# Kernel optimization log

Measured on AMD Instinct MI355X. Metric: run time of the kernel, lower is better.

The kernel has to match this reference:

```python
import jax, jax.numpy as jnp
import numpy as np

# dims: B batch, S src len, D input_size, H rnn hidden, E embedding_dim,
# V = output_size + 2 (vocab + Start/End), T = max target len (+2 for Start/End)
B, S, D, H, E, V, T = 128, 512, 256, 512, 256, 1002, 34
END = V - 1  # 'End' token index


def _gru_layer(x, h0, Wih, Whh, bih, bhh):
    """PyTorch-convention GRU layer. x: [B,T,Din], h0: [B,H].
    Wih: [3H,Din], Whh: [3H,H]. Returns (outputs [B,T,H], h_T [B,H])."""
    def step(h, xt):
        gi = xt @ Wih.T + bih            # [B,3H]
        gh = h @ Whh.T + bhh             # [B,3H]
        i_r, i_z, i_n = jnp.split(gi, 3, axis=-1)
        h_r, h_z, h_n = jnp.split(gh, 3, axis=-1)
        r = jax.nn.sigmoid(i_r + h_r)
        z = jax.nn.sigmoid(i_z + h_z)
        n = jnp.tanh(i_n + r * h_n)
        h_new = (1.0 - z) * n + z * h
        return h_new, h_new
    hT, ys = jax.lax.scan(step, h0, jnp.swapaxes(x, 0, 1))
    return jnp.swapaxes(ys, 0, 1), hT


def _gru_stack(x, h0s, layers):
    """h0s: [L,B,H]; layers: list of (Wih,Whh,bih,bhh). Returns (out, h [L,B,H])."""
    hs = []
    y = x
    for l, (Wih, Whh, bih, bhh) in enumerate(layers):
        y, hT = _gru_layer(y, h0s[l], Wih, Whh, bih, bhh)
        hs.append(hT)
    return y, jnp.stack(hs, axis=0)


def setup_inputs() -> dict:
    key = jax.random.key(0)
    ks = jax.random.split(key, 32)
    sc = 0.05
    inp = {}
    inp['source'] = jax.random.normal(ks[0], (B, S, D), dtype=jnp.float32)
    inp['target_ids'] = jax.random.randint(ks[1], (B, T), 0, V)
    inp['lengths'] = jax.random.randint(ks[2], (B,), 2, T + 1)
    inp['emb'] = sc * jax.random.normal(ks[3], (V, E), dtype=jnp.float32)
    # encoder layer 0 (in=D) and layer 1 (in=H)
    inp['enc_Wih0'] = sc * jax.random.normal(ks[4], (3 * H, D), dtype=jnp.float32)
    inp['enc_Whh0'] = sc * jax.random.normal(ks[5], (3 * H, H), dtype=jnp.float32)
    inp['enc_bih0'] = jnp.zeros((3 * H,), jnp.float32)
    inp['enc_bhh0'] = jnp.zeros((3 * H,), jnp.float32)
    inp['enc_Wih1'] = sc * jax.random.normal(ks[6], (3 * H, H), dtype=jnp.float32)
    inp['enc_Whh1'] = sc * jax.random.normal(ks[7], (3 * H, H), dtype=jnp.float32)
    inp['enc_bih1'] = jnp.zeros((3 * H,), jnp.float32)
    inp['enc_bhh1'] = jnp.zeros((3 * H,), jnp.float32)
    # decoder layer 0 (in=E) and layer 1 (in=H)
    inp['dec_Wih0'] = sc * jax.random.normal(ks[8], (3 * H, E), dtype=jnp.float32)
    inp['dec_Whh0'] = sc * jax.random.normal(ks[9], (3 * H, H), dtype=jnp.float32)
    inp['dec_bih0'] = jnp.zeros((3 * H,), jnp.float32)
    inp['dec_bhh0'] = jnp.zeros((3 * H,), jnp.float32)
    inp['dec_Wih1'] = sc * jax.random.normal(ks[10], (3 * H, H), dtype=jnp.float32)
    inp['dec_Whh1'] = sc * jax.random.normal(ks[11], (3 * H, H), dtype=jnp.float32)
    inp['dec_bih1'] = jnp.zeros((3 * H,), jnp.float32)
    inp['dec_bhh1'] = jnp.zeros((3 * H,), jnp.float32)
    # fc: H -> 5H -> 2H -> V
    inp['fc_W1'] = sc * jax.random.normal(ks[12], (5 * H, H), dtype=jnp.float32)
    inp['fc_b1'] = jnp.zeros((5 * H,), jnp.float32)
    inp['fc_W2'] = sc * jax.random.normal(ks[13], (2 * H, 5 * H), dtype=jnp.float32)
    inp['fc_b2'] = jnp.zeros((2 * H,), jnp.float32)
    inp['fc_W3'] = sc * jax.random.normal(ks[14], (V, 2 * H), dtype=jnp.float32)
    inp['fc_b3'] = jnp.zeros((V,), jnp.float32)
    return inp


def reference(source, target_ids, lengths, emb,
              enc_Wih0, enc_Whh0, enc_bih0, enc_bhh0,
              enc_Wih1, enc_Whh1, enc_bih1, enc_bhh1,
              dec_Wih0, dec_Whh0, dec_bih0, dec_bhh0,
              dec_Wih1, dec_Whh1, dec_bih1, dec_bhh1,
              fc_W1, fc_b1, fc_W2, fc_b2, fc_W3, fc_b3):
    Bx = source.shape[0]
    h0 = jnp.zeros((2, Bx, H), source.dtype)
    # encoder: only final hidden state h [L,B,H] is used
    _, h = _gru_stack(source, h0,
                      [(enc_Wih0, enc_Whh0, enc_bih0, enc_bhh0),
                       (enc_Wih1, enc_Whh1, enc_bih1, enc_bhh1)])
    # decoder over embedded (Start + target + End + pad) sequences
    tg = emb[target_ids]                               # [B,T,E]
    out, _ = _gru_stack(tg, h,
                        [(dec_Wih0, dec_Whh0, dec_bih0, dec_bhh0),
                         (dec_Wih1, dec_Whh1, dec_bih1, dec_bhh1)])
    # pad_packed_sequence zeroes timesteps >= length; sum over time
    mask = (jnp.arange(T)[None, :] < lengths[:, None]).astype(out.dtype)  # [B,T]
    pooled = jnp.einsum('bth,bt->bh', out, mask)       # [B,H]
    x = pooled @ fc_W1.T + fc_b1
    x = x @ fc_W2.T + fc_b2
    x = x @ fc_W3.T + fc_b3
    scores = jax.nn.sigmoid(x)                         # [B,V]
    # CrossEntropyLoss against the 'End' index for every row
    logp = jax.nn.log_softmax(scores, axis=-1)
    loss = -jnp.mean(logp[:, END])
    return loss
```

## Files before the change

kernel.cpp:

```cpp
#include <hip/hip_runtime.h>
#include <hip/hip_bf16.h>
#include <math.h>

#define B_ 128
#define S_ 512
#define D_ 256
#define H_ 512
#define E_ 256
#define V_ 1002
#define T_ 34
#define END_ 1001
#define NWG_TOTAL 128
#define HROWB 1040
#define GPITCH 20

typedef __attribute__((ext_vector_type(8))) short short8;
typedef __attribute__((ext_vector_type(4))) float f32x4;
typedef __attribute__((ext_vector_type(4))) int i32x4;
typedef unsigned long long u64;

__device__ __forceinline__ float bf2f(unsigned short u){
  union { unsigned int i; float f; } x; x.i = ((unsigned int)u) << 16; return x.f;
}
__device__ __forceinline__ unsigned short f2bf(float f){
  union { float f; unsigned int i; } x; x.f = f;
  unsigned int r = x.i + 0x7fffu + ((x.i >> 16) & 1u);
  return (unsigned short)(r >> 16);
}
__device__ __forceinline__ float sigm(float x){ return 1.0f / (1.0f + expf(-x)); }

__device__ __forceinline__ void store_coh8(unsigned short* p, u64 v){
  __hip_atomic_store((u64*)p, v, __ATOMIC_RELAXED, __HIP_MEMORY_SCOPE_AGENT);
}

__device__ __forceinline__ i32x4 load_flags16(const unsigned* p){
  i32x4 r;
  asm volatile("global_load_dwordx4 %0, %1, off sc0 sc1\n\ts_waitcnt vmcnt(0)"
               : "=v"(r) : "v"(p) : "memory");
  return r;
}

__device__ __forceinline__ void stage_tile_coh(const unsigned short* src, char* dst, int tid){
  i32x4 r[16];
  #pragma unroll
  for (int p = 0; p < 16; ++p){
    const char* sp = (const char*)src + p * 4096 + tid * 16;
    asm volatile("global_load_dwordx4 %0, %1, off sc0 sc1" : "=v"(r[p]) : "v"(sp));
  }
  asm volatile("s_waitcnt vmcnt(0)" ::: "memory");
  #pragma unroll
  for (int p = 0; p < 16; ++p){
    const int off = p * 4096 + tid * 16;
    *reinterpret_cast<i32x4*>(dst + (off >> 10) * HROWB + (off & 1023)) = r[p];
  }
}


__global__ void f2bf_kernel(const float* __restrict__ in, unsigned short* __restrict__ out, int n){
  int i = blockIdx.x * blockDim.x + threadIdx.x;
  int stride = gridDim.x * blockDim.x;
  for (; i < n; i += stride) out[i] = f2bf(in[i]);
}

__global__ void embed_kernel(const float* __restrict__ emb, const int* __restrict__ ids,
                             unsigned short* __restrict__ out){
  int i = blockIdx.x * blockDim.x + threadIdx.x;
  if (i >= B_ * T_ * E_) return;
  int bt = i >> 8;
  int e  = i & (E_ - 1);
  out[i] = f2bf(emb[(size_t)ids[bt] * E_ + e]);
}

__global__ void build_wcat(const float* __restrict__ Wih, const float* __restrict__ Whh,
                           unsigned short* __restrict__ Wcat, int Din){
  int K = Din + H_;
  int total = 2048 * K;
  int i = blockIdx.x * blockDim.x + threadIdx.x;
  int stride = gridDim.x * blockDim.x;
  for (; i < total; i += stride){
    int n = i / K, k = i - n * K;
    int g = n >> 9, j = n & 511;
    float v;
    if (g < 2){
      int r = (g << 9) + j;
      v = (k < Din) ? Wih[(size_t)r * Din + k] : Whh[(size_t)r * H_ + (k - Din)];
    } else if (g == 2){
      v = (k < Din) ? Wih[(size_t)(1024 + j) * Din + k] : 0.0f;
    } else {
      v = (k < Din) ? 0.0f : Whh[(size_t)(1024 + j) * H_ + (k - Din)];
    }
    Wcat[i] = f2bf(v);
  }
}

__global__ void build_bias(const float* __restrict__ bih, const float* __restrict__ bhh,
                           float* __restrict__ out){
  int j = blockIdx.x * blockDim.x + threadIdx.x;
  if (j >= 512) return;
  out[j]        = bih[j] + bhh[j];
  out[512 + j]  = bih[512 + j] + bhh[512 + j];
  out[1024 + j] = bih[1024 + j];
  out[1536 + j] = bhh[1024 + j];
}


template<int KT, int XKT>
__device__ __forceinline__ void run_layer(
    char* smem,
    const unsigned short* __restrict__ Wc, const float* __restrict__ bias4,
    const unsigned short* __restrict__ Xbase, int x_rs, int x_ts,
    unsigned short* Ybase,
    unsigned short* hb0, unsigned short* hb1,
    int T, unsigned round0,
    unsigned* own_flags, int slot,
    unsigned* prod_flags, unsigned prod0,
    u64* hprev,
    int jtile, int mh, int wv, int lane)
{
  constexpr int K   = KT * 32;
  constexpr int KTL = KT / 4;
  const int tid  = threadIdx.x;
  const int ln   = lane & 15;
  const int lk8  = (lane >> 4) << 3;
  const int base_m = mh * 64;
  const int q = wv;

  char*  hA   = smem;
  float* gbuf = (float*)(smem + 64 * HROWB);

  short8 wreg[4][KTL];
  #pragma unroll
  for (int g = 0; g < 4; ++g)
    #pragma unroll
    for (int k = 0; k < KTL; ++k)
      wreg[g][k] = *reinterpret_cast<const short8*>(
          Wc + (size_t)(g * 512 + jtile * 16 + ln) * K + (size_t)(q * KTL + k) * 32 + lk8);

  const int erow  = tid >> 2;
  const int ecol0 = (tid & 3) << 2;
  const int ej    = (jtile << 4) + ecol0;
  const int egr   = base_m + erow;
  f32x4 bR, bZ, bNI, bNH;
  #pragma unroll
  for (int c = 0; c < 4; ++c){
    bR[c]  = bias4[ej + c];
    bZ[c]  = bias4[512 + ej + c];
    bNI[c] = bias4[1024 + ej + c];
    bNH[c] = bias4[1536 + ej + c];
  }

  for (int t = 0; t < T; ++t){
    if (wv == 0){
      const unsigned own_t  = round0 + (unsigned)t;
      const unsigned prod_t = prod0 + (unsigned)t + 1u;
      const unsigned* pofs = own_flags + (lane & 7) * 4;
      const unsigned* ppfs = prod_flags ? (prod_flags + (lane & 7) * 4) : nullptr;
      for (;;){
        i32x4 f = load_flags16(pofs);
        bool ok = (unsigned)f.x >= own_t && (unsigned)f.y >= own_t &&
                  (unsigned)f.z >= own_t && (unsigned)f.w >= own_t;
        if (ppfs){
          i32x4 g = load_flags16(ppfs);
          ok = ok && (unsigned)g.x >= prod_t && (unsigned)g.y >= prod_t &&
                     (unsigned)g.z >= prod_t && (unsigned)g.w >= prod_t;
        }
        if (__all(ok)) break;
        __builtin_amdgcn_s_sleep(1);
      }
    }
    __syncthreads();

    const unsigned short* Hin  = (t & 1) ? hb1 : hb0;
    unsigned short*       Hout = (t & 1) ? hb0 : hb1;
    const unsigned short* Xt   = Xbase + (size_t)t * x_ts;

    stage_tile_coh(Hin + ((size_t)base_m << 9), hA, tid);
    __syncthreads();

    f32x4 acc[4][4];
    #pragma unroll
    for (int g = 0; g < 4; ++g)
      #pragma unroll
      for (int mt = 0; mt < 4; ++mt) acc[g][mt] = (f32x4){0.f, 0.f, 0.f, 0.f};

    #pragma unroll
    for (int k = 0; k < KTL; ++k){
      const int kt = q * KTL + k;
      short8 a[4];
      if (kt < XKT){
        #pragma unroll
        for (int mt = 0; mt < 4; ++mt)
          a[mt] = *reinterpret_cast<const short8*>(
              Xt + (size_t)(base_m + mt * 16 + ln) * x_rs + kt * 32 + lk8);
      } else {
        #pragma unroll
        for (int mt = 0; mt < 4; ++mt)
          a[mt] = *reinterpret_cast<const short8*>(
              hA + (mt * 16 + ln) * HROWB + ((kt - XKT) * 32 + lk8) * 2);
      }
      #pragma unroll
      for (int g = 0; g < 4; ++g)
        #pragma unroll
        for (int mt = 0; mt < 4; ++mt)
          acc[g][mt] = __builtin_amdgcn_mfma_f32_16x16x32_bf16(a[mt], wreg[g][k], acc[g][mt], 0, 0, 0);
    }

    #pragma unroll
    for (int g = 0; g < 4; ++g)
      #pragma unroll
      for (int mt = 0; mt < 4; ++mt){
        const int rl = mt * 16 + ((lane >> 4) << 2);
        #pragma unroll
        for (int i = 0; i < 4; ++i)
          gbuf[((q * 4 + g) * 64 + rl + i) * GPITCH + ln] = acc[g][mt][i];
      }
    __syncthreads();

    {
      f32x4 p0 = (f32x4){0.f,0.f,0.f,0.f}, p1 = p0, p2 = p0, p3 = p0;
      #pragma unroll
      for (int qq = 0; qq < 4; ++qq){
        p0 += *reinterpret_cast<const f32x4*>(gbuf + ((qq * 4 + 0) * 64 + erow) * GPITCH + ecol0);
        p1 += *reinterpret_cast<const f32x4*>(gbuf + ((qq * 4 + 1) * 64 + erow) * GPITCH + ecol0);
        p2 += *reinterpret_cast<const f32x4*>(gbuf + ((qq * 4 + 2) * 64 + erow) * GPITCH + ecol0);
        p3 += *reinterpret_cast<const f32x4*>(gbuf + ((qq * 4 + 3) * 64 + erow) * GPITCH + ecol0);
      }
      u64 hv = *hprev;
      u64 hb = 0;
      #pragma unroll
      for (int c = 0; c < 4; ++c){
        float rr = sigm(p0[c] + bR[c]);
        float zz = sigm(p1[c] + bZ[c]);
        float nn = tanhf(p2[c] + bNI[c] + rr * (p3[c] + bNH[c]));
        float hp = bf2f((unsigned short)(hv >> (16 * c)));
        float hn = (1.0f - zz) * nn + zz * hp;
        hb |= ((u64)f2bf(hn)) << (16 * c);
      }
      *hprev = hb;
      store_coh8(Hout + ((size_t)egr << 9) + ej, hb);
      if (Ybase)
        store_coh8(Ybase + (size_t)t * (B_ * H_) + ((size_t)egr << 9) + ej, hb);
    }

    asm volatile("s_waitcnt vmcnt(0)" ::: "memory");
    __syncthreads();
    if (tid == 0)
      __hip_atomic_store(own_flags + slot, round0 + (unsigned)t + 1u,
                         __ATOMIC_RELAXED, __HIP_MEMORY_SCOPE_AGENT);
  }
}

__global__ __launch_bounds__(256, 1)
void rnn_persistent(
    const unsigned short* __restrict__ src, const unsigned short* __restrict__ tg,
    const unsigned short* __restrict__ Wc_e0, const unsigned short* __restrict__ Wc_e1,
    const unsigned short* __restrict__ Wc_d0, const unsigned short* __restrict__ Wc_d1,
    const float* __restrict__ b_e0, const float* __restrict__ b_e1,
    const float* __restrict__ b_d0, const float* __restrict__ b_d1,
    unsigned short* h0a, unsigned short* h0b,
    unsigned short* h1a, unsigned short* h1b,
    unsigned short* y0, unsigned short* z0, unsigned short* y1,
    unsigned* flags)
{
  __shared__ __align__(16) char smem[64 * HROWB + 16 * 64 * GPITCH * 4];
  __builtin_amdgcn_fence(__ATOMIC_ACQUIRE, "agent");
  const int wg = blockIdx.x;
  const int layer = wg >> 6;
  const int gidx = wg & 63;
  const int jtile = gidx & 31, mh = gidx >> 5;
  const int wv = threadIdx.x >> 6, lane = threadIdx.x & 63;
  unsigned* own  = flags + (size_t)((layer << 1) | mh) * 64;
  unsigned* prod = flags + (size_t)mh * 64;
  u64 hprev = 0;
  if (layer == 0){
    run_layer<24, 8>(smem, Wc_e0, b_e0, src, S_ * D_, D_, y0,
                     h0a, h0b, S_, 0u, own, jtile, nullptr, 0u, &hprev,
                     jtile, mh, wv, lane);
    run_layer<24, 8>(smem, Wc_d0, b_d0, tg, T_ * E_, E_, z0,
                     h0a, h0b, T_, 512u, own, jtile, nullptr, 0u, &hprev,
                     jtile, mh, wv, lane);
  } else {
    run_layer<32, 16>(smem, Wc_e1, b_e1, y0, H_, B_ * H_, (unsigned short*)nullptr,
                      h1a, h1b, S_, 0u, own, jtile, prod, 0u, &hprev,
                      jtile, mh, wv, lane);
    run_layer<32, 16>(smem, Wc_d1, b_d1, z0, H_, B_ * H_, y1,
                      h1a, h1b, T_, 512u, own, jtile, prod, 512u, &hprev,
                      jtile, mh, wv, lane);
  }
}

__global__ __launch_bounds__(256)
void gemm_nt(const unsigned short* __restrict__ A, const unsigned short* __restrict__ W,
             const float* __restrict__ bias,
             unsigned short* __restrict__ outB, float* __restrict__ outF,
             int M, int N, int K, int act)
{
  const int w    = threadIdx.x >> 6;
  const int lane = threadIdx.x & 63;
  const int ln   = lane & 15;
  const int lk8  = (lane >> 4) << 3;
  const int row0 = blockIdx.y * 32;
  const int col0 = blockIdx.x * 256 + w * 64;

  f32x4 acc[2][4];
  #pragma unroll
  for (int a = 0; a < 2; a++)
    #pragma unroll
    for (int g = 0; g < 4; g++) acc[a][g] = (f32x4){0.f, 0.f, 0.f, 0.f};

  const unsigned short* arow0 = A + (size_t)(row0 + ln) * K;
  const unsigned short* arow1 = A + (size_t)(row0 + 16 + ln) * K;
  const unsigned short* wrow[4];
  int ncol[4];
  #pragma unroll
  for (int nt = 0; nt < 4; ++nt){
    int n = col0 + nt * 16 + ln;
    ncol[nt] = n;
    int nc = n < N ? n : (N - 1);
    wrow[nt] = W + (size_t)nc * K;
  }

  const int nk = K >> 5;
  for (int kt = 0; kt < nk; ++kt){
    const int k = (kt << 5) + lk8;
    short8 a0 = *reinterpret_cast<const short8*>(arow0 + k);
    short8 a1 = *reinterpret_cast<const short8*>(arow1 + k);
    #pragma unroll
    for (int nt = 0; nt < 4; ++nt){
      short8 bf = *reinterpret_cast<const short8*>(wrow[nt] + k);
      acc[0][nt] = __builtin_amdgcn_mfma_f32_16x16x32_bf16(a0, bf, acc[0][nt], 0, 0, 0);
      acc[1][nt] = __builtin_amdgcn_mfma_f32_16x16x32_bf16(a1, bf, acc[1][nt], 0, 0, 0);
    }
  }

  #pragma unroll
  for (int nt = 0; nt < 4; ++nt){
    const int n = ncol[nt];
    if (n >= N) continue;
    const float bv = bias ? bias[n] : 0.0f;
    #pragma unroll
    for (int mt = 0; mt < 2; ++mt){
      const int rbase = row0 + mt * 16 + ((lane >> 4) << 2);
      #pragma unroll
      for (int reg = 0; reg < 4; ++reg){
        const int row = rbase + reg;
        if (row >= M) continue;
        float v = acc[mt][nt][reg] + bv;
        if (act == 1) v = sigm(v);
        if (outB) outB[(size_t)row * N + n] = f2bf(v);
        if (outF) outF[(size_t)row * N + n] = v;
      }
    }
  }
}


__global__ void pool_kernel(const unsigned short* __restrict__ y1, const int* __restrict__ lengths,
                            unsigned short* __restrict__ pooled){
  int i = blockIdx.x * blockDim.x + threadIdx.x;
  if (i >= B_ * H_) return;
  int b = i >> 9;
  int j = i & (H_ - 1);
  int len = lengths[b]; if (len > T_) len = T_;
  float s = 0.0f;
  for (int t = 0; t < len; ++t) s += bf2f(y1[((size_t)t * B_ + b) * H_ + j]);
  pooled[i] = f2bf(s);
}

__global__ void loss_kernel(const float* __restrict__ scores, float* __restrict__ out){
  __shared__ float wsum[4];
  const int w = threadIdx.x >> 6;
  const int lane = threadIdx.x & 63;
  float acc = 0.0f;
  for (int b = w; b < B_; b += 4){
    const float* row = scores + (size_t)b * V_;
    float vals[16];
    float mx = -1e30f;
    #pragma unroll
    for (int i = 0; i < 16; ++i){
      int c = lane + i * 64;
      vals[i] = (c < V_) ? row[c] : -1e30f;
      mx = fmaxf(mx, vals[i]);
    }
    #pragma unroll
    for (int off = 32; off; off >>= 1) mx = fmaxf(mx, __shfl_xor(mx, off));
    float se = 0.0f;
    #pragma unroll
    for (int i = 0; i < 16; ++i){
      int c = lane + i * 64;
      if (c < V_) se += expf(vals[i] - mx);
    }
    #pragma unroll
    for (int off = 32; off; off >>= 1) se += __shfl_xor(se, off);
    float logp = row[END_] - (mx + logf(se));
    acc += logp;
  }
  if (lane == 0) wsum[w] = acc;
  __syncthreads();
  if (threadIdx.x == 0){
    out[0] = -(wsum[0] + wsum[1] + wsum[2] + wsum[3]) / (float)B_;
  }
}


extern "C" void kernel_launch(void* const* d_in, const int* in_sizes, int n_in,
                              void* d_out, int out_size, void* d_ws, size_t ws_size,
                              hipStream_t stream) {
  const float* source   = (const float*)d_in[0];
  const int*   tgt_ids  = (const int*)  d_in[1];
  const int*   lengths  = (const int*)  d_in[2];
  const float* emb      = (const float*)d_in[3];
  const float* eWih0 = (const float*)d_in[4],  *eWhh0 = (const float*)d_in[5];
  const float* ebih0 = (const float*)d_in[6],  *ebhh0 = (const float*)d_in[7];
  const float* eWih1 = (const float*)d_in[8],  *eWhh1 = (const float*)d_in[9];
  const float* ebih1 = (const float*)d_in[10], *ebhh1 = (const float*)d_in[11];
  const float* dWih0 = (const float*)d_in[12], *dWhh0 = (const float*)d_in[13];
  const float* dbih0 = (const float*)d_in[14], *dbhh0 = (const float*)d_in[15];
  const float* dWih1 = (const float*)d_in[16], *dWhh1 = (const float*)d_in[17];
  const float* dbih1 = (const float*)d_in[18], *dbhh1 = (const float*)d_in[19];
  const float* fcW1 = (const float*)d_in[20], *fcb1 = (const float*)d_in[21];
  const float* fcW2 = (const float*)d_in[22], *fcb2 = (const float*)d_in[23];
  const float* fcW3 = (const float*)d_in[24], *fcb3 = (const float*)d_in[25];

  char* p = (char*)d_ws;
  auto alloc = [&](size_t bytes) -> void* {
    void* r = (void*)p;
    p += (bytes + 255) & ~(size_t)255;
    return r;
  };

  unsigned short* src_bf = (unsigned short*)alloc((size_t)B_ * S_ * D_ * 2);
  unsigned short* tg_bf  = (unsigned short*)alloc((size_t)B_ * T_ * E_ * 2);
  unsigned short* y0_bf  = (unsigned short*)alloc((size_t)S_ * B_ * H_ * 2);
  unsigned short* z0d    = (unsigned short*)alloc((size_t)T_ * B_ * H_ * 2);
  unsigned short* y1d    = (unsigned short*)alloc((size_t)T_ * B_ * H_ * 2);
  unsigned short* h0a = (unsigned short*)alloc((size_t)B_ * H_ * 2);
  unsigned short* h0b = (unsigned short*)alloc((size_t)B_ * H_ * 2);
  unsigned short* h1a = (unsigned short*)alloc((size_t)B_ * H_ * 2);
  unsigned short* h1b = (unsigned short*)alloc((size_t)B_ * H_ * 2);
  unsigned short* Wc_e0 = (unsigned short*)alloc((size_t)2048 * 768  * 2);
  unsigned short* Wc_e1 = (unsigned short*)alloc((size_t)2048 * 1024 * 2);
  unsigned short* Wc_d0 = (unsigned short*)alloc((size_t)2048 * 768  * 2);
  unsigned short* Wc_d1 = (unsigned short*)alloc((size_t)2048 * 1024 * 2);
  float* bias_e0 = (float*)alloc(2048 * 4);
  float* bias_e1 = (float*)alloc(2048 * 4);
  float* bias_d0 = (float*)alloc(2048 * 4);
  float* bias_d1 = (float*)alloc(2048 * 4);
  unsigned short* fcW1b = (unsigned short*)alloc((size_t)2560 * 512  * 2);
  unsigned short* fcW2b = (unsigned short*)alloc((size_t)1024 * 2560 * 2);
  unsigned short* fcW3b = (unsigned short*)alloc((size_t)V_ * 1024 * 2);
  unsigned short* pooled = (unsigned short*)alloc((size_t)B_ * H_ * 2);
  unsigned short* x1_bf  = (unsigned short*)alloc((size_t)B_ * 2560 * 2);
  unsigned short* x2_bf  = (unsigned short*)alloc((size_t)B_ * 1024 * 2);
  float* scores = (float*)alloc((size_t)B_ * V_ * 4);
  unsigned* flags = (unsigned*)alloc(4 * 64 * 4);

  f2bf_kernel<<<8192, 256, 0, stream>>>(source, src_bf, B_ * S_ * D_);
  embed_kernel<<<(B_ * T_ * E_ + 255) / 256, 256, 0, stream>>>(emb, tgt_ids, tg_bf);
  build_wcat<<<2048, 256, 0, stream>>>(eWih0, eWhh0, Wc_e0, D_);
  build_wcat<<<2048, 256, 0, stream>>>(eWih1, eWhh1, Wc_e1, H_);
  build_wcat<<<2048, 256, 0, stream>>>(dWih0, dWhh0, Wc_d0, E_);
  build_wcat<<<2048, 256, 0, stream>>>(dWih1, dWhh1, Wc_d1, H_);
  build_bias<<<2, 256, 0, stream>>>(ebih0, ebhh0, bias_e0);
  build_bias<<<2, 256, 0, stream>>>(ebih1, ebhh1, bias_e1);
  build_bias<<<2, 256, 0, stream>>>(dbih0, dbhh0, bias_d0);
  build_bias<<<2, 256, 0, stream>>>(dbih1, dbhh1, bias_d1);
  f2bf_kernel<<<4096, 256, 0, stream>>>(fcW1, fcW1b, 2560 * 512);
  f2bf_kernel<<<4096, 256, 0, stream>>>(fcW2, fcW2b, 1024 * 2560);
  f2bf_kernel<<<4096, 256, 0, stream>>>(fcW3, fcW3b, V_ * 1024);

  hipMemsetAsync(h0a, 0, (size_t)B_ * H_ * 2, stream);
  hipMemsetAsync(h0b, 0, (size_t)B_ * H_ * 2, stream);
  hipMemsetAsync(h1a, 0, (size_t)B_ * H_ * 2, stream);
  hipMemsetAsync(h1b, 0, (size_t)B_ * H_ * 2, stream);
  hipMemsetAsync(flags, 0, 4 * 64 * 4, stream);

  rnn_persistent<<<NWG_TOTAL, 256, 0, stream>>>(
      src_bf, tg_bf, Wc_e0, Wc_e1, Wc_d0, Wc_d1,
      bias_e0, bias_e1, bias_d0, bias_d1,
      h0a, h0b, h1a, h1b, y0_bf, z0d, y1d, flags);

  pool_kernel<<<(B_ * H_ + 255) / 256, 256, 0, stream>>>(y1d, lengths, pooled);

  {
    dim3 g1((2560 + 255) / 256, B_ / 32);
    gemm_nt<<<g1, 256, 0, stream>>>(pooled, fcW1b, fcb1, x1_bf, (float*)nullptr,
                                    B_, 2560, 512, 0);
    dim3 g2((1024 + 255) / 256, B_ / 32);
    gemm_nt<<<g2, 256, 0, stream>>>(x1_bf, fcW2b, fcb2, x2_bf, (float*)nullptr,
                                    B_, 1024, 2560, 0);
    dim3 g3((V_ + 255) / 256, B_ / 32);
    gemm_nt<<<g3, 256, 0, stream>>>(x2_bf, fcW3b, fcb3, (unsigned short*)nullptr, scores,
                                    B_, V_, 1024, 1);
  }

  loss_kernel<<<1, 256, 0, stream>>>(scores, (float*)d_out);
}
```

Before: 4.387 ms.

## Store full hidden-state history and read recurrent state directly from global

Replaces the two ping-pong hidden buffers and separate layer-output buffers with one time-indexed history buffer per layer. Each timestep now writes one fresh location, which serves as both the next recurrent input and the layer output. Because every step reads addresses that were never read before, the MFMA loop can load the previous hidden state straight from global memory with ordinary loads. This removes the coherent LDS staging copy and one barrier per step, and the duplicate Y store is dropped. In exchange it uses much larger buffers and depends on plain loads not returning stale cached data.

```diff
diff --git a/kernel.cpp b/kernel.cpp
--- a/kernel.cpp
+++ b/kernel.cpp
@@ -11,7 +11,7 @@
 #define T_ 34
 #define END_ 1001
 #define NWG_TOTAL 128
-#define HROWB 1040
+#define BH (B_ * H_)
 #define GPITCH 20
 
 typedef __attribute__((ext_vector_type(8))) short short8;
@@ -38,21 +38,6 @@
   asm volatile("global_load_dwordx4 %0, %1, off sc0 sc1\n\ts_waitcnt vmcnt(0)"
                : "=v"(r) : "v"(p) : "memory");
   return r;
-}
-
-__device__ __forceinline__ void stage_tile_coh(const unsigned short* src, char* dst, int tid){
-  i32x4 r[16];
-  #pragma unroll
-  for (int p = 0; p < 16; ++p){
-    const char* sp = (const char*)src + p * 4096 + tid * 16;
-    asm volatile("global_load_dwordx4 %0, %1, off sc0 sc1" : "=v"(r[p]) : "v"(sp));
-  }
-  asm volatile("s_waitcnt vmcnt(0)" ::: "memory");
-  #pragma unroll
-  for (int p = 0; p < 16; ++p){
-    const int off = p * 4096 + tid * 16;
-    *reinterpret_cast<i32x4*>(dst + (off >> 10) * HROWB + (off & 1023)) = r[p];
-  }
 }
 
 
@@ -106,11 +91,11 @@
 
 template<int KT, int XKT>
 __device__ __forceinline__ void run_layer(
-    char* smem,
+    float* gbuf,
     const unsigned short* __restrict__ Wc, const float* __restrict__ bias4,
     const unsigned short* __restrict__ Xbase, int x_rs, int x_ts,
-    unsigned short* Ybase,
-    unsigned short* hb0, unsigned short* hb1,
+    const unsigned short* __restrict__ Hread,
+    unsigned short* Hwrite,
     int T, unsigned round0,
     unsigned* own_flags, int slot,
     unsigned* prod_flags, unsigned prod0,
@@ -124,9 +109,6 @@
   const int lk8  = (lane >> 4) << 3;
   const int base_m = mh * 64;
   const int q = wv;
-
-  char*  hA   = smem;
-  float* gbuf = (float*)(smem + 64 * HROWB);
 
   short8 wreg[4][KTL];
   #pragma unroll
@@ -170,12 +152,8 @@
     }
     __syncthreads();
 
-    const unsigned short* Hin  = (t & 1) ? hb1 : hb0;
-    unsigned short*       Hout = (t & 1) ? hb0 : hb1;
-    const unsigned short* Xt   = Xbase + (size_t)t * x_ts;
-
-    stage_tile_coh(Hin + ((size_t)base_m << 9), hA, tid);
-    __syncthreads();
+    const unsigned short* Xt  = Xbase + (size_t)t * x_ts;
+    const unsigned short* Hin = Hread + (size_t)t * BH;
 
     f32x4 acc[4][4];
     #pragma unroll
@@ -196,7 +174,7 @@
         #pragma unroll
         for (int mt = 0; mt < 4; ++mt)
           a[mt] = *reinterpret_cast<const short8*>(
-              hA + (mt * 16 + ln) * HROWB + ((kt - XKT) * 32 + lk8) * 2);
+              Hin + (size_t)(base_m + mt * 16 + ln) * H_ + (kt - XKT) * 32 + lk8);
       }
       #pragma unroll
       for (int g = 0; g < 4; ++g)
@@ -237,9 +215,7 @@
         hb |= ((u64)f2bf(hn)) << (16 * c);
       }
       *hprev = hb;
-      store_coh8(Hout + ((size_t)egr << 9) + ej, hb);
-      if (Ybase)
-        store_coh8(Ybase + (size_t)t * (B_ * H_) + ((size_t)egr << 9) + ej, hb);
+      store_coh8(Hwrite + (size_t)t * BH + ((size_t)egr << 9) + ej, hb);
     }
 
     asm volatile("s_waitcnt vmcnt(0)" ::: "memory");
@@ -257,12 +233,10 @@
     const unsigned short* __restrict__ Wc_d0, const unsigned short* __restrict__ Wc_d1,
     const float* __restrict__ b_e0, const float* __restrict__ b_e1,
     const float* __restrict__ b_d0, const float* __restrict__ b_d1,
-    unsigned short* h0a, unsigned short* h0b,
-    unsigned short* h1a, unsigned short* h1b,
-    unsigned short* y0, unsigned short* z0, unsigned short* y1,
+    unsigned short* H0, unsigned short* H1,
     unsigned* flags)
 {
-  __shared__ __align__(16) char smem[64 * HROWB + 16 * 64 * GPITCH * 4];
+  __shared__ __align__(16) float gbuf[16 * 64 * GPITCH];
   __builtin_amdgcn_fence(__ATOMIC_ACQUIRE, "agent");
   const int wg = blockIdx.x;
   const int layer = wg >> 6;
@@ -273,18 +247,20 @@
   unsigned* prod = flags + (size_t)mh * 64;
   u64 hprev = 0;
   if (layer == 0){
-    run_layer<24, 8>(smem, Wc_e0, b_e0, src, S_ * D_, D_, y0,
-                     h0a, h0b, S_, 0u, own, jtile, nullptr, 0u, &hprev,
+    run_layer<24, 8>(gbuf, Wc_e0, b_e0, src, S_ * D_, D_,
+                     H0, H0 + BH, S_, 0u, own, jtile, nullptr, 0u, &hprev,
                      jtile, mh, wv, lane);
-    run_layer<24, 8>(smem, Wc_d0, b_d0, tg, T_ * E_, E_, z0,
-                     h0a, h0b, T_, 512u, own, jtile, nullptr, 0u, &hprev,
+    run_layer<24, 8>(gbuf, Wc_d0, b_d0, tg, T_ * E_, E_,
+                     H0 + (size_t)512 * BH, H0 + (size_t)513 * BH, T_, 512u,
+                     own, jtile, nullptr, 0u, &hprev,
                      jtile, mh, wv, lane);
   } else {
-    run_layer<32, 16>(smem, Wc_e1, b_e1, y0, H_, B_ * H_, (unsigned short*)nullptr,
-                      h1a, h1b, S_, 0u, own, jtile, prod, 0u, &hprev,
+    run_layer<32, 16>(gbuf, Wc_e1, b_e1, H0 + BH, H_, BH,
+                      H1, H1 + BH, S_, 0u, own, jtile, prod, 0u, &hprev,
                       jtile, mh, wv, lane);
-    run_layer<32, 16>(smem, Wc_d1, b_d1, z0, H_, B_ * H_, y1,
-                      h1a, h1b, T_, 512u, own, jtile, prod, 512u, &hprev,
+    run_layer<32, 16>(gbuf, Wc_d1, b_d1, H0 + (size_t)513 * BH, H_, BH,
+                      H1 + (size_t)512 * BH, H1 + (size_t)513 * BH, T_, 512u,
+                      own, jtile, prod, 512u, &hprev,
                       jtile, mh, wv, lane);
   }
 }
@@ -355,7 +331,7 @@
 }
 
 
-__global__ void pool_kernel(const unsigned short* __restrict__ y1, const int* __restrict__ lengths,
+__global__ void pool_kernel(const unsigned short* __restrict__ H1, const int* __restrict__ lengths,
                             unsigned short* __restrict__ pooled){
   int i = blockIdx.x * blockDim.x + threadIdx.x;
   if (i >= B_ * H_) return;
@@ -363,7 +339,8 @@
   int j = i & (H_ - 1);
   int len = lengths[b]; if (len > T_) len = T_;
   float s = 0.0f;
-  for (int t = 0; t < len; ++t) s += bf2f(y1[((size_t)t * B_ + b) * H_ + j]);
+  for (int t = 0; t < len; ++t)
+    s += bf2f(H1[(size_t)(513 + t) * BH + ((size_t)b << 9) + j]);
   pooled[i] = f2bf(s);
 }
 
@@ -431,13 +408,8 @@
 
   unsigned short* src_bf = (unsigned short*)alloc((size_t)B_ * S_ * D_ * 2);
   unsigned short* tg_bf  = (unsigned short*)alloc((size_t)B_ * T_ * E_ * 2);
-  unsigned short* y0_bf  = (unsigned short*)alloc((size_t)S_ * B_ * H_ * 2);
-  unsigned short* z0d    = (unsigned short*)alloc((size_t)T_ * B_ * H_ * 2);
-  unsigned short* y1d    = (unsigned short*)alloc((size_t)T_ * B_ * H_ * 2);
-  unsigned short* h0a = (unsigned short*)alloc((size_t)B_ * H_ * 2);
-  unsigned short* h0b = (unsigned short*)alloc((size_t)B_ * H_ * 2);
-  unsigned short* h1a = (unsigned short*)alloc((size_t)B_ * H_ * 2);
-  unsigned short* h1b = (unsigned short*)alloc((size_t)B_ * H_ * 2);
+  unsigned short* H0 = (unsigned short*)alloc((size_t)547 * BH * 2);
+  unsigned short* H1 = (unsigned short*)alloc((size_t)547 * BH * 2);
   unsigned short* Wc_e0 = (unsigned short*)alloc((size_t)2048 * 768  * 2);
   unsigned short* Wc_e1 = (unsigned short*)alloc((size_t)2048 * 1024 * 2);
   unsigned short* Wc_d0 = (unsigned short*)alloc((size_t)2048 * 768  * 2);
@@ -469,18 +441,16 @@
   f2bf_kernel<<<4096, 256, 0, stream>>>(fcW2, fcW2b, 1024 * 2560);
   f2bf_kernel<<<4096, 256, 0, stream>>>(fcW3, fcW3b, V_ * 1024);
 
-  hipMemsetAsync(h0a, 0, (size_t)B_ * H_ * 2, stream);
-  hipMemsetAsync(h0b, 0, (size_t)B_ * H_ * 2, stream);
-  hipMemsetAsync(h1a, 0, (size_t)B_ * H_ * 2, stream);
-  hipMemsetAsync(h1b, 0, (size_t)B_ * H_ * 2, stream);
+  hipMemsetAsync(H0, 0, (size_t)BH * 2, stream);
+  hipMemsetAsync(H1, 0, (size_t)BH * 2, stream);
   hipMemsetAsync(flags, 0, 4 * 64 * 4, stream);
 
   rnn_persistent<<<NWG_TOTAL, 256, 0, stream>>>(
       src_bf, tg_bf, Wc_e0, Wc_e1, Wc_d0, Wc_d1,
       bias_e0, bias_e1, bias_d0, bias_d1,
-      h0a, h0b, h1a, h1b, y0_bf, z0d, y1d, flags);
-
-  pool_kernel<<<(B_ * H_ + 255) / 256, 256, 0, stream>>>(y1d, lengths, pooled);
+      H0, H1, flags);
+
+  pool_kernel<<<(B_ * H_ + 255) / 256, 256, 0, stream>>>(H1, lengths, pooled);
 
   {
     dim3 g1((2560 + 255) / 256, B_ / 32);
```

Result: slower. 4.923 ms (+12.2%).
